# Kernel optimization log

Measured on AMD Instinct MI355X. Metric: run time of the kernel, lower is better.

The kernel has to match this reference:

```python
import jax, jax.numpy as jnp
import numpy as np

B, S, D, H, W, L, V = 4, 8192, 256, 8, 64, 6, 256
DH = D // H          # head dim 32
NW = S // W          # number of windows
FF = 4 * D


def setup_inputs() -> dict:
    key = jax.random.key(0)
    ks = jax.random.split(key, 12)
    w = lambda k, shape: (jax.random.normal(k, shape, jnp.float32) * 0.02)
    return {
        "input_ids": jax.random.randint(ks[0], (B, S), 0, V).astype(jnp.int32),
        "attention_mask": jnp.ones((B, S), jnp.int32),
        "word_start": jax.random.randint(ks[1], (B, S), 0, 2).astype(jnp.int32),
        "emb": w(ks[2], (V, D)),
        "pos_emb": w(ks[3], (S, D)),
        "ln1_g": jnp.ones((L, D)), "ln1_b": jnp.zeros((L, D)),
        "wq": w(ks[4], (L, D, D)), "wk": w(ks[5], (L, D, D)),
        "wv": w(ks[6], (L, D, D)), "wo": w(ks[7], (L, D, D)),
        "ln2_g": jnp.ones((L, D)), "ln2_b": jnp.zeros((L, D)),
        "w1": w(ks[8], (L, D, FF)), "b1": jnp.zeros((L, FF)),
        "w2": w(ks[9], (L, FF, D)), "b2": jnp.zeros((L, D)),
        "lnf_g": jnp.ones((D,)), "lnf_b": jnp.zeros((D,)),
    }


def _ln(x, g, b):
    m = jnp.mean(x, -1, keepdims=True)
    v = jnp.mean((x - m) ** 2, -1, keepdims=True)
    return (x - m) * jax.lax.rsqrt(v + 1e-5) * g + b


def _local_attn(x, mask_bool, wq, wk, wv, wo):
    # non-causal local attention: each 64-token window attends to
    # [prev window, own window, next window] (look_backward=1, look_forward=1)
    def heads(t):
        return t.reshape(B, S, H, DH).transpose(0, 2, 1, 3)  # [B,H,S,DH]
    q = heads(x @ wq)
    k = heads(x @ wk)
    v = heads(x @ wv)
    qw = q.reshape(B, H, NW, W, DH)

    def ctx(t):  # gather 3-window key/value context
        tw = t.reshape(B, H, NW, W, DH)
        tp = jnp.pad(tw, ((0, 0), (0, 0), (1, 1), (0, 0), (0, 0)))
        return jnp.concatenate([tp[:, :, i:i + NW] for i in range(3)], axis=3)  # [B,H,NW,3W,DH]

    kc, vc = ctx(k), ctx(v)
    mw = mask_bool.reshape(B, NW, W)
    mp = jnp.pad(mw, ((0, 0), (1, 1), (0, 0)))
    mc = jnp.concatenate([mp[:, i:i + NW] for i in range(3)], axis=2)  # [B,NW,3W]

    scores = jnp.einsum('bhnwd,bhnkd->bhnwk', qw, kc) * (DH ** -0.5)
    scores = jnp.where(mc[:, None, :, None, :], scores, -1e9)
    attn = jax.nn.softmax(scores, axis=-1)
    o = jnp.einsum('bhnwk,bhnkd->bhnwd', attn, vc)
    o = o.reshape(B, H, S, DH).transpose(0, 2, 1, 3).reshape(B, S, D)
    return o @ wo


def _gather_word_starts(x, ws):
    # pack hidden states at word-start positions to the front, zero-padded
    def one(xb, wb):
        idx = jnp.cumsum(wb) - 1
        tgt = jnp.where(wb > 0, idx, S)  # invalid rows go to scratch slot S
        return jnp.zeros((S + 1, xb.shape[-1]), xb.dtype).at[tgt].set(xb)[:S]
    return jax.vmap(one)(x, ws)


def reference(input_ids, attention_mask, word_start, emb, pos_emb,
              ln1_g, ln1_b, wq, wk, wv, wo, ln2_g, ln2_b,
              w1, b1, w2, b2, lnf_g, lnf_b):
    mask_bool = attention_mask > 0
    x = emb[input_ids] + pos_emb[None, :, :]
    for i in range(L):
        x = x + _local_attn(_ln(x, ln1_g[i], ln1_b[i]), mask_bool,
                            wq[i], wk[i], wv[i], wo[i])
        h = _ln(x, ln2_g[i], ln2_b[i])
        x = x + jax.nn.gelu(h @ w1[i] + b1[i]) @ w2[i] + b2[i]
    x = _ln(x, lnf_g, lnf_b)
    return _gather_word_starts(x, word_start)
```

## Files before the change

### kernel.cpp

```cpp
#include <hip/hip_runtime.h>


#define S_LEN 8192
#define BATCH 4
#define DMODEL 256
#define NHEAD 8
#define WIN 64
#define NWIN 128
#define NLAYER 6
#define FFDIM 1024
#define MROWS (BATCH * S_LEN)

typedef float __attribute__((ext_vector_type(4))) f32x4;
typedef unsigned int __attribute__((ext_vector_type(2))) u32x2;
typedef unsigned short u16;
typedef unsigned short __attribute__((ext_vector_type(4))) u16x4;

__device__ __forceinline__ u16 f2bf(float f) {
  unsigned u = __builtin_bit_cast(unsigned, f);
  u += 0x7fffu + ((u >> 16) & 1u);
  return (u16)(u >> 16);
}

__device__ __forceinline__ unsigned cvt_pk_bf16(float lo, float hi) {
  unsigned r;
  asm("v_cvt_pk_bf16_f32 %0, %1, %2" : "=v"(r) : "v"(lo), "v"(hi));
  return r;
}
__device__ __forceinline__ u32x2 pack_bf16x4(f32x4 v) {
  u32x2 o;
  o[0] = cvt_pk_bf16(v[0], v[1]);
  o[1] = cvt_pk_bf16(v[2], v[3]);
  return o;
}
__device__ __forceinline__ f32x4 unpack_bf16x4(u16x4 h) {
  f32x4 o;
  o[0] = __builtin_bit_cast(float, (unsigned)h[0] << 16);
  o[1] = __builtin_bit_cast(float, (unsigned)h[1] << 16);
  o[2] = __builtin_bit_cast(float, (unsigned)h[2] << 16);
  o[3] = __builtin_bit_cast(float, (unsigned)h[3] << 16);
  return o;
}

__device__ __forceinline__ float exp2_f(float x) {
  float r;
  asm("v_exp_f32 %0, %1" : "=v"(r) : "v"(x));
  return r;
}

__device__ __forceinline__ void mfma16(f32x4& d, f32x4 a, f32x4 b) {
  asm volatile("v_mfma_f32_16x16x32_bf16 %0, %1, %2, %0"
               : "+v"(d) : "v"(a), "v"(b));
}
#define MFMA_FENCE() asm volatile("s_nop 7\n\ts_nop 7")

__device__ __forceinline__ void gload_lds16(const void* g, void* l) {
  __builtin_amdgcn_global_load_lds(
      (__attribute__((address_space(1))) void*)g,
      (__attribute__((address_space(3))) void*)l, 16, 0, 0);
}

__device__ __forceinline__ float gelu_f(float t) {
  float u = 0.7978845608028654f * (t + 0.044715f * t * t * t);
  float e = __expf(-2.0f * u);
  return t * __builtin_amdgcn_rcpf(1.0f + e);
}

__global__ __launch_bounds__(256) void embed_ln_kernel(
    const int* __restrict__ ids, const float* __restrict__ emb,
    const float* __restrict__ pos, const float* __restrict__ g,
    const float* __restrict__ b, u16* __restrict__ x, u16* __restrict__ xb) {
  int wid = threadIdx.x >> 6, lane = threadIdx.x & 63;
  int r = blockIdx.x * 4 + wid;
  int s = r & (S_LEN - 1);
  int id = ids[r];
  f32x4 e = *(const f32x4*)(emb + (size_t)id * DMODEL + lane * 4);
  f32x4 p = *(const f32x4*)(pos + (size_t)s * DMODEL + lane * 4);
  f32x4 v = e + p;
  *(u32x2*)(x + (size_t)r * DMODEL + lane * 4) = pack_bf16x4(v);
  float sm = v[0] + v[1] + v[2] + v[3];
  float q = v[0] * v[0] + v[1] * v[1] + v[2] * v[2] + v[3] * v[3];
  for (int off = 32; off; off >>= 1) {
    sm += __shfl_xor(sm, off, 64);
    q += __shfl_xor(q, off, 64);
  }
  float mean = sm * (1.0f / DMODEL);
  float var = q * (1.0f / DMODEL) - mean * mean;
  float rs = rsqrtf(var + 1e-5f);
  f32x4 gg = *(const f32x4*)(g + lane * 4);
  f32x4 bb = *(const f32x4*)(b + lane * 4);
  f32x4 o;
  for (int j = 0; j < 4; ++j) o[j] = (v[j] - mean) * rs * gg[j] + bb[j];
  *(u32x2*)(xb + (size_t)r * DMODEL + lane * 4) = pack_bf16x4(o);
}

__global__ void zero_kernel(float* __restrict__ p, int n4) {
  int i = blockIdx.x * blockDim.x + threadIdx.x;
  int stride = gridDim.x * blockDim.x;
  f32x4 z = {0.f, 0.f, 0.f, 0.f};
  for (; i < n4; i += stride) ((f32x4*)p)[i] = z;
}

__global__ void tcast_kernel(const float* __restrict__ src, u16* __restrict__ dst,
                             int total, int K, int N, int dls, int rowOff) {
  int i = blockIdx.x * blockDim.x + threadIdx.x;
  int stride = gridDim.x * blockDim.x;
  int KN = K * N;
  for (; i < total; i += stride) {
    int l = i / KN;
    int rem = i - l * KN;
    int k = rem / N;
    int n = rem - k * N;
    dst[l * dls + (rowOff + n) * K + k] = f2bf(src[i]);
  }
}

template <bool GELU_ACT, bool HAS_BIAS, bool QKV>
__global__ __launch_bounds__(256) void gemm_bf16(
    const u16* __restrict__ A, const u16* __restrict__ Bt,
    u16* __restrict__ C, u16* __restrict__ Vt, const float* __restrict__ bias,
    int N, int K, int nx) {
  __shared__ u16 As[128 * 64];
  __shared__ u16 Bs[128 * 64];

  int nwg = gridDim.x;
  int bid = blockIdx.x;
  int w8 = (bid & 7) * (nwg >> 3) + (bid >> 3);
  int cx = w8 % nx, ry = w8 / nx;
  int bm = ry * 128, bn = cx * 128;

  int tid = threadIdx.x, lane = tid & 63, wid = tid >> 6;
  int l15 = lane & 15, l4 = lane >> 4;
  int wm = wid >> 1, wn = wid & 1;

  const u16* Ab = A + (size_t)bm * K;
  const u16* Bb = Bt + (size_t)bn * K;

  f32x4 acc[4][4] = {};

  for (int kt = 0; kt < K; kt += 64) {
#pragma unroll
    for (int i = 0; i < 4; ++i) {
      int s = tid + i * 256;
      int r = s >> 3, c = (s & 7) ^ (r & 7);
      gload_lds16(Ab + (size_t)r * K + kt + c * 8,
                  (char*)As + (wid * 64 + i * 256) * 16);
    }
#pragma unroll
    for (int i = 0; i < 4; ++i) {
      int s = tid + i * 256;
      int r = s >> 3, c = (s & 7) ^ (r & 7);
      gload_lds16(Bb + (size_t)r * K + kt + c * 8,
                  (char*)Bs + (wid * 64 + i * 256) * 16);
    }
    __syncthreads();
#pragma unroll
    for (int t = 0; t < 2; ++t) {
      f32x4 af[4], bf[4];
#pragma unroll
      for (int m = 0; m < 4; ++m) {
        int r = wm * 64 + m * 16 + l15;
        af[m] = ((const f32x4*)As)[r * 8 + ((t * 4 + l4) ^ (r & 7))];
      }
#pragma unroll
      for (int n = 0; n < 4; ++n) {
        int r = wn * 64 + n * 16 + l15;
        bf[n] = ((const f32x4*)Bs)[r * 8 + ((t * 4 + l4) ^ (r & 7))];
      }
#pragma unroll
      for (int m = 0; m < 4; ++m)
#pragma unroll
        for (int n = 0; n < 4; ++n) mfma16(acc[m][n], bf[n], af[m]);
    }
    __syncthreads();
  }
  MFMA_FENCE();

  int colB = bn + wn * 64;
  if (QKV && colB >= 512) {
#pragma unroll
    for (int m = 0; m < 4; ++m) {
      int row = bm + wm * 64 + m * 16 + l15;
      int bb = row >> 13, s = row & (S_LEN - 1);
#pragma unroll
      for (int n = 0; n < 4; ++n)
#pragma unroll
        for (int j = 0; j < 4; ++j) {
          int col = colB + n * 16 + l4 * 4 + j;
          Vt[((size_t)(bb * 256 + (col - 512))) * S_LEN + s] =
              f2bf(acc[m][n][j]);
        }
    }
    return;
  }
  f32x4 bv[4];
#pragma unroll
  for (int n = 0; n < 4; ++n)
    bv[n] = HAS_BIAS ? *(const f32x4*)(bias + colB + n * 16 + l4 * 4)
                     : (f32x4){0.f, 0.f, 0.f, 0.f};
#pragma unroll
  for (int m = 0; m < 4; ++m) {
    int row = bm + wm * 64 + m * 16 + l15;
#pragma unroll
    for (int n = 0; n < 4; ++n) {
      f32x4 v = acc[m][n] + bv[n];
      if (GELU_ACT) {
#pragma unroll
        for (int j = 0; j < 4; ++j) v[j] = gelu_f(v[j]);
      }
      *(u32x2*)(C + (size_t)row * N + colB + n * 16 + l4 * 4) = pack_bf16x4(v);
    }
  }
}

template <bool DO_LN>
__global__ __launch_bounds__(256) void gemm_res_ln(
    const u16* __restrict__ A, const u16* __restrict__ Bt,
    u16* __restrict__ x, u16* __restrict__ xb,
    const float* __restrict__ bias, const float* __restrict__ g,
    const float* __restrict__ b, int K) {
  __shared__ u16 As[64 * 64];
  __shared__ u16 Bs[256 * 64];
  __shared__ float redS[64][4];
  __shared__ float redQ[64][4];

  int nwg = gridDim.x;
  int bid = blockIdx.x;
  int bm = ((bid & 7) * (nwg >> 3) + (bid >> 3)) * 64;

  int tid = threadIdx.x, lane = tid & 63, wid = tid >> 6;
  int l15 = lane & 15, l4 = lane >> 4;

  const u16* Ab = A + (size_t)bm * K;
  f32x4 acc[4][4] = {};

  for (int kt = 0; kt < K; kt += 64) {
#pragma unroll
    for (int i = 0; i < 2; ++i) {
      int s = tid + i * 256;
      int r = s >> 3, c = (s & 7) ^ (r & 7);
      gload_lds16(Ab + (size_t)r * K + kt + c * 8,
                  (char*)As + (wid * 64 + i * 256) * 16);
    }
#pragma unroll
    for (int i = 0; i < 8; ++i) {
      int s = tid + i * 256;
      int r = s >> 3, c = (s & 7) ^ (r & 7);
      gload_lds16(Bt + (size_t)r * K + kt + c * 8,
                  (char*)Bs + (wid * 64 + i * 256) * 16);
    }
    __syncthreads();
#pragma unroll
    for (int t = 0; t < 2; ++t) {
      f32x4 af[4], bf[4];
#pragma unroll
      for (int m = 0; m < 4; ++m) {
        int r = m * 16 + l15;
        af[m] = ((const f32x4*)As)[r * 8 + ((t * 4 + l4) ^ (r & 7))];
      }
#pragma unroll
      for (int n = 0; n < 4; ++n) {
        int r = wid * 64 + n * 16 + l15;
        bf[n] = ((const f32x4*)Bs)[r * 8 + ((t * 4 + l4) ^ (r & 7))];
      }
#pragma unroll
      for (int m = 0; m < 4; ++m)
#pragma unroll
        for (int n = 0; n < 4; ++n) mfma16(acc[m][n], bf[n], af[m]);
    }
    __syncthreads();
  }
  MFMA_FENCE();

  int colB = wid * 64;
  f32x4 bv[4];
#pragma unroll
  for (int n = 0; n < 4; ++n)
    bv[n] = bias ? *(const f32x4*)(bias + colB + n * 16 + l4 * 4)
                 : (f32x4){0.f, 0.f, 0.f, 0.f};

#pragma unroll
  for (int m = 0; m < 4; ++m) {
    int r = m * 16 + l15;
    size_t rowoff = (size_t)(bm + r) * DMODEL + colB;
    float s = 0.f, q = 0.f;
#pragma unroll
    for (int n = 0; n < 4; ++n) {
      f32x4 xv = unpack_bf16x4(*(const u16x4*)(x + rowoff + n * 16 + l4 * 4));
      f32x4 v = acc[m][n] + bv[n] + xv;
      acc[m][n] = v;
      s += v[0] + v[1] + v[2] + v[3];
      q += v[0] * v[0] + v[1] * v[1] + v[2] * v[2] + v[3] * v[3];
    }
    if (DO_LN) {
      s += __shfl_xor(s, 16, 64);
      s += __shfl_xor(s, 32, 64);
      q += __shfl_xor(q, 16, 64);
      q += __shfl_xor(q, 32, 64);
      if (l4 == 0) {
        redS[r][wid] = s;
        redQ[r][wid] = q;
      }
    }
  }
  if (DO_LN) __syncthreads();

  f32x4 gv[4], bbv[4];
  if (DO_LN) {
#pragma unroll
    for (int n = 0; n < 4; ++n) {
      gv[n] = *(const f32x4*)(g + colB + n * 16 + l4 * 4);
      bbv[n] = *(const f32x4*)(b + colB + n * 16 + l4 * 4);
    }
  }
#pragma unroll
  for (int m = 0; m < 4; ++m) {
    int r = m * 16 + l15;
    size_t rowoff = (size_t)(bm + r) * DMODEL + colB;
    float mean = 0.f, rs = 0.f;
    if (DO_LN) {
      f32x4 sv = *(const f32x4*)redS[r];
      f32x4 qv = *(const f32x4*)redQ[r];
      float ssum = sv[0] + sv[1] + sv[2] + sv[3];
      float qsum = qv[0] + qv[1] + qv[2] + qv[3];
      mean = ssum * (1.0f / DMODEL);
      float var = qsum * (1.0f / DMODEL) - mean * mean;
      rs = rsqrtf(var + 1e-5f);
    }
#pragma unroll
    for (int n = 0; n < 4; ++n) {
      f32x4 v = acc[m][n];
      *(u32x2*)(x + rowoff + n * 16 + l4 * 4) = pack_bf16x4(v);
      if (DO_LN) {
        f32x4 o;
#pragma unroll
        for (int j = 0; j < 4; ++j)
          o[j] = (v[j] - mean) * rs * gv[n][j] + bbv[n][j];
        *(u32x2*)(xb + rowoff + n * 16 + l4 * 4) = pack_bf16x4(o);
      }
    }
  }
}

__global__ __launch_bounds__(256, 4) void attn_kernel(
    const u16* __restrict__ qkv, const u16* __restrict__ vt,
    const int* __restrict__ amask, u16* __restrict__ ao) {
  int win = blockIdx.x, h = blockIdx.y, b = blockIdx.z;
  int tid = threadIdx.x, lane = tid & 63, wid = tid >> 6;
  int l15 = lane & 15, l4 = lane >> 4;

  __shared__ u16 KPs[192 * 64];
  __shared__ u16 Vts[96 * 64];
  __shared__ float bias[192];

  int t0 = win * WIN - WIN;

  if (tid < 192) {
    int t = t0 + tid;
    bias[tid] =
        (t >= 0 && t < S_LEN && amask[b * S_LEN + t] != 0) ? 0.0f : -1e9f;
  }
#pragma unroll
  for (int it = 0; it < 3; ++it) {
    int c = it * 256 + tid;
    int k = c >> 2, j = c & 3;
    int t = t0 + k;
    t = t < 0 ? 0 : (t >= S_LEN ? S_LEN - 1 : t);
    f32x4 kd = *(const f32x4*)(qkv + (size_t)(b * S_LEN + t) * 768 + 256 +
                               h * 32 + j * 8);
    int row = k >> 1;
    int cc = (((k & 1) << 2) | j) ^ (row & 7);
    *(f32x4*)(KPs + row * 64 + cc * 8) = kd;
  }
#pragma unroll
  for (int it = 0; it < 3; ++it) {
    int c = it * 256 + tid;
    int d = c / 24, kc = c - d * 24;
    int ts = t0 + kc * 8;
    ts = ts < 0 ? 0 : (ts > S_LEN - 8 ? S_LEN - 8 : ts);
    f32x4 vd = *(const f32x4*)(vt + ((size_t)((b * 8 + h) * 32 + d)) * S_LEN + ts);
    int row = d * 3 + (kc >> 3);
    int cc = (kc & 7) ^ (row & 7);
    *(f32x4*)(Vts + row * 64 + cc * 8) = vd;
  }
  __syncthreads();

  int qrow = b * S_LEN + win * WIN + wid * 16 + l15;
  f32x4 aq = *(const f32x4*)(qkv + (size_t)qrow * 768 + h * 32 + l4 * 8);

  f32x4 sacc[12] = {};
  int krb = l15 >> 1;
  int kcc = (((l15 & 1) << 2) | l4) ^ (krb & 7);
#pragma unroll
  for (int f = 0; f < 12; ++f) {
    f32x4 bk = *(const f32x4*)(KPs + (f * 8 + krb) * 64 + kcc * 8);
    mfma16(sacc[f], bk, aq);
  }
  MFMA_FENCE();

  const float scale2 = 0.17677669529663687f * 1.4426950408889634f;
  float mrow = -1e30f;
#pragma unroll
  for (int f = 0; f < 12; ++f) {
    f32x4 bi = *(const f32x4*)&bias[f * 16 + l4 * 4];
#pragma unroll
    for (int j = 0; j < 4; ++j) {
      float sv = fmaf(sacc[f][j], scale2, bi[j]);
      sacc[f][j] = sv;
      mrow = fmaxf(mrow, sv);
    }
  }
  mrow = fmaxf(mrow, __shfl_xor(mrow, 16, 64));
  mrow = fmaxf(mrow, __shfl_xor(mrow, 32, 64));

  float ssum = 0.f;
#pragma unroll
  for (int f = 0; f < 12; ++f)
#pragma unroll
    for (int j = 0; j < 4; ++j) {
      float p = exp2_f(sacc[f][j] - mrow);
      sacc[f][j] = p;
      ssum += p;
    }
  ssum += __shfl_xor(ssum, 16, 64);
  ssum += __shfl_xor(ssum, 32, 64);

  __syncthreads();

  int q = wid * 16 + l15;
#pragma unroll
  for (int f = 0; f < 12; ++f) {
    u32x2 pk;
    pk[0] = cvt_pk_bf16(sacc[f][0], sacc[f][1]);
    pk[1] = cvt_pk_bf16(sacc[f][2], sacc[f][3]);
    int kc = f * 2 + (l4 >> 1);
    int row = q * 3 + (kc >> 3);
    int cc = (kc & 7) ^ (row & 7);
    *(u32x2*)(KPs + row * 64 + cc * 8 + (l4 & 1) * 4) = pk;
  }
  __syncthreads();

  f32x4 oacc[2] = {};
#pragma unroll
  for (int kk = 0; kk < 6; ++kk) {
    int kc = kk * 4 + l4;
    int rowp = q * 3 + (kc >> 3);
    int ccp = (kc & 7) ^ (rowp & 7);
    f32x4 ap = *(const f32x4*)(KPs + rowp * 64 + ccp * 8);
#pragma unroll
    for (int nf = 0; nf < 2; ++nf) {
      int d = nf * 16 + l15;
      int rowv = d * 3 + (kc >> 3);
      int ccv = (kc & 7) ^ (rowv & 7);
      f32x4 bvv = *(const f32x4*)(Vts + rowv * 64 + ccv * 8);
      mfma16(oacc[nf], bvv, ap);
    }
  }
  MFMA_FENCE();

  float invv = 1.0f / ssum;
  size_t obase = (size_t)qrow * 256 + h * 32;
#pragma unroll
  for (int nf = 0; nf < 2; ++nf) {
    f32x4 v = oacc[nf] * invv;
    *(u32x2*)(ao + obase + nf * 16 + l4 * 4) = pack_bf16x4(v);
  }
}

__global__ __launch_bounds__(256) void scan_kernel(const int* __restrict__ wsrt,
                                                   int* __restrict__ tgt) {
  __shared__ int part[256];
  int b = blockIdx.x, tid = threadIdx.x;
  const int* src = wsrt + b * S_LEN;
  int* dst = tgt + b * S_LEN;
  int base = tid * 32;
  int loc[32];
  int s = 0;
#pragma unroll
  for (int i = 0; i < 32; ++i) {
    loc[i] = src[base + i];
    s += loc[i];
  }
  part[tid] = s;
  __syncthreads();
  for (int off = 1; off < 256; off <<= 1) {
    int v = (tid >= off) ? part[tid - off] : 0;
    __syncthreads();
    part[tid] += v;
    __syncthreads();
  }
  int cum = part[tid] - s;
#pragma unroll
  for (int i = 0; i < 32; ++i) {
    cum += loc[i];
    dst[base + i] = (loc[i] > 0) ? (cum - 1) : -1;
  }
}

__global__ __launch_bounds__(64) void gather_ln_kernel(
    const u16* __restrict__ x, const int* __restrict__ tgt,
    const float* __restrict__ g, const float* __restrict__ b,
    float* __restrict__ out) {
  int r = blockIdx.x;
  int tg = tgt[r];
  if (tg < 0) return;
  int bIdx = r >> 13;
  int lane = threadIdx.x;
  f32x4 v = unpack_bf16x4(*(const u16x4*)(x + (size_t)r * DMODEL + lane * 4));
  float s = v[0] + v[1] + v[2] + v[3];
  float q = v[0] * v[0] + v[1] * v[1] + v[2] * v[2] + v[3] * v[3];
  for (int off = 32; off; off >>= 1) {
    s += __shfl_xor(s, off, 64);
    q += __shfl_xor(q, off, 64);
  }
  float mean = s * (1.0f / DMODEL);
  float var = q * (1.0f / DMODEL) - mean * mean;
  float rs = rsqrtf(var + 1e-5f);
  f32x4 gg = *(const f32x4*)(g + lane * 4);
  f32x4 bb = *(const f32x4*)(b + lane * 4);
  f32x4 o;
  for (int j = 0; j < 4; ++j) o[j] = (v[j] - mean) * rs * gg[j] + bb[j];
  *(f32x4*)(out + (size_t)(bIdx * S_LEN + tg) * DMODEL + lane * 4) = o;
}

extern "C" void kernel_launch(void* const* d_in, const int* in_sizes, int n_in,
                              void* d_out, int out_size, void* d_ws,
                              size_t ws_size, hipStream_t stream) {
  const int* ids = (const int*)d_in[0];
  const int* amask = (const int*)d_in[1];
  const int* wstart = (const int*)d_in[2];
  const float* emb = (const float*)d_in[3];
  const float* pos = (const float*)d_in[4];
  const float* ln1g = (const float*)d_in[5];
  const float* ln1b = (const float*)d_in[6];
  const float* wq = (const float*)d_in[7];
  const float* wk = (const float*)d_in[8];
  const float* wv = (const float*)d_in[9];
  const float* wo = (const float*)d_in[10];
  const float* ln2g = (const float*)d_in[11];
  const float* ln2b = (const float*)d_in[12];
  const float* w1 = (const float*)d_in[13];
  const float* b1 = (const float*)d_in[14];
  const float* w2 = (const float*)d_in[15];
  const float* b2 = (const float*)d_in[16];
  const float* lnfg = (const float*)d_in[17];
  const float* lnfb = (const float*)d_in[18];

  char* ws = (char*)d_ws;
  const size_t OFF_X = 0;
  const size_t OFF_XB = 33554432;
  const size_t OFF_AO = 50331648;
  const size_t OFF_BIG = 67108864;
  const size_t OFF_VT = 117440512;
  const size_t OFF_WQKVT = 134217728;
  const size_t OFF_WOT = 136577024;
  const size_t OFF_W1T = 137363456;
  const size_t OFF_W2T = 140509184;
  const size_t OFF_TGT = 143654912;
  const size_t NEEDED = 143785984;
  if (ws_size < NEEDED) return;

  u16* x = (u16*)(ws + OFF_X);
  u16* xb = (u16*)(ws + OFF_XB);
  u16* ao = (u16*)(ws + OFF_AO);
  u16* big = (u16*)(ws + OFF_BIG);
  u16* vt = (u16*)(ws + OFF_VT);
  u16* WqkvT = (u16*)(ws + OFF_WQKVT);
  u16* WoT = (u16*)(ws + OFF_WOT);
  u16* W1T = (u16*)(ws + OFF_W1T);
  u16* W2T = (u16*)(ws + OFF_W2T);
  int* tgt = (int*)(ws + OFF_TGT);

  tcast_kernel<<<1024, 256, 0, stream>>>(wq, WqkvT, NLAYER * 256 * 256, 256, 256, 768 * 256, 0);
  tcast_kernel<<<1024, 256, 0, stream>>>(wk, WqkvT, NLAYER * 256 * 256, 256, 256, 768 * 256, 256);
  tcast_kernel<<<1024, 256, 0, stream>>>(wv, WqkvT, NLAYER * 256 * 256, 256, 256, 768 * 256, 512);
  tcast_kernel<<<1024, 256, 0, stream>>>(wo, WoT, NLAYER * 256 * 256, 256, 256, 256 * 256, 0);
  tcast_kernel<<<2048, 256, 0, stream>>>(w1, W1T, NLAYER * 256 * 1024, 256, 1024, 1024 * 256, 0);
  tcast_kernel<<<2048, 256, 0, stream>>>(w2, W2T, NLAYER * 1024 * 256, 1024, 256, 256 * 1024, 0);

  embed_ln_kernel<<<MROWS / 4, 256, 0, stream>>>(ids, emb, pos, ln1g, ln1b, x, xb);
  zero_kernel<<<2048, 256, 0, stream>>>((float*)d_out, out_size / 4);
  scan_kernel<<<BATCH, 256, 0, stream>>>(wstart, tgt);

  for (int l = 0; l < NLAYER; ++l) {
    gemm_bf16<false, false, true><<<1536, 256, 0, stream>>>(
        xb, WqkvT + (size_t)l * 768 * 256, big, vt, nullptr, 768, 256, 6);
    attn_kernel<<<dim3(NWIN, NHEAD, BATCH), 256, 0, stream>>>(big, vt, amask, ao);
    gemm_res_ln<true><<<MROWS / 64, 256, 0, stream>>>(
        ao, WoT + (size_t)l * 256 * 256, x, xb, nullptr,
        ln2g + l * DMODEL, ln2b + l * DMODEL, 256);
    gemm_bf16<true, true, false><<<2048, 256, 0, stream>>>(
        xb, W1T + (size_t)l * 1024 * 256, big, nullptr, b1 + l * FFDIM, 1024, 256, 8);
    if (l < NLAYER - 1) {
      gemm_res_ln<true><<<MROWS / 64, 256, 0, stream>>>(
          big, W2T + (size_t)l * 256 * 1024, x, xb, b2 + l * DMODEL,
          ln1g + (l + 1) * DMODEL, ln1b + (l + 1) * DMODEL, 1024);
    } else {
      gemm_res_ln<false><<<MROWS / 64, 256, 0, stream>>>(
          big, W2T + (size_t)l * 256 * 1024, x, nullptr, b2 + l * DMODEL,
          nullptr, nullptr, 1024);
    }
  }

  gather_ln_kernel<<<MROWS, 64, 0, stream>>>(x, tgt, lnfg, lnfb, (float*)d_out);
}
```

Before: 856.9 us.

## Fuse FFN up-projection, GELU and down-projection into one kernel

Replaces the separate W1 GEMM (with bias and GELU) and the W2 GEMM plus residual/LayerNorm with a single ffn_fused kernel. Each 64-row block keeps its input rows in registers and computes the 1024-wide hidden activation in 128-column chunks in LDS. Each chunk is fed straight into the W2 accumulation, so the large hidden tensor never goes through global memory. In exchange, every block re-streams the full W1 and W2 weights from cache and runs with many barriers and no double buffering. The QKV GEMM template is also simplified into a dedicated kernel.

```diff
diff --git a/kernel.cpp b/kernel.cpp
--- a/kernel.cpp
+++ b/kernel.cpp
@@ -115,11 +115,9 @@
   }
 }
 
-template <bool GELU_ACT, bool HAS_BIAS, bool QKV>
-__global__ __launch_bounds__(256) void gemm_bf16(
+__global__ __launch_bounds__(256) void qkv_gemm(
     const u16* __restrict__ A, const u16* __restrict__ Bt,
-    u16* __restrict__ C, u16* __restrict__ Vt, const float* __restrict__ bias,
-    int N, int K, int nx) {
+    u16* __restrict__ C, u16* __restrict__ Vt, int N, int K, int nx) {
   __shared__ u16 As[128 * 64];
   __shared__ u16 Bs[128 * 64];
 
@@ -177,7 +175,7 @@
   MFMA_FENCE();
 
   int colB = bn + wn * 64;
-  if (QKV && colB >= 512) {
+  if (colB >= 512) {
 #pragma unroll
     for (int m = 0; m < 4; ++m) {
       int row = bm + wm * 64 + m * 16 + l15;
@@ -193,23 +191,13 @@
     }
     return;
   }
-  f32x4 bv[4];
-#pragma unroll
-  for (int n = 0; n < 4; ++n)
-    bv[n] = HAS_BIAS ? *(const f32x4*)(bias + colB + n * 16 + l4 * 4)
-                     : (f32x4){0.f, 0.f, 0.f, 0.f};
 #pragma unroll
   for (int m = 0; m < 4; ++m) {
     int row = bm + wm * 64 + m * 16 + l15;
 #pragma unroll
-    for (int n = 0; n < 4; ++n) {
-      f32x4 v = acc[m][n] + bv[n];
-      if (GELU_ACT) {
-#pragma unroll
-        for (int j = 0; j < 4; ++j) v[j] = gelu_f(v[j]);
-      }
-      *(u32x2*)(C + (size_t)row * N + colB + n * 16 + l4 * 4) = pack_bf16x4(v);
-    }
+    for (int n = 0; n < 4; ++n)
+      *(u32x2*)(C + (size_t)row * N + colB + n * 16 + l4 * 4) =
+          pack_bf16x4(acc[m][n]);
   }
 }
 
@@ -337,6 +325,178 @@
         for (int j = 0; j < 4; ++j)
           o[j] = (v[j] - mean) * rs * gv[n][j] + bbv[n][j];
         *(u32x2*)(xb + rowoff + n * 16 + l4 * 4) = pack_bf16x4(o);
+      }
+    }
+  }
+}
+
+template <bool DO_LN>
+__global__ __launch_bounds__(256) void ffn_fused(
+    const u16* __restrict__ xbin, const u16* __restrict__ W1t,
+    const u16* __restrict__ W2t, const float* __restrict__ b1,
+    const float* __restrict__ b2, u16* __restrict__ x,
+    u16* __restrict__ xbout, const float* __restrict__ g,
+    const float* __restrict__ b) {
+  __shared__ u16 Ws[256 * 64];
+  __shared__ u16 Hs[64 * 128];
+  __shared__ float redS[64][4];
+  __shared__ float redQ[64][4];
+
+  int nwg = gridDim.x;
+  int bid = blockIdx.x;
+  int bm = ((bid & 7) * (nwg >> 3) + (bid >> 3)) * 64;
+
+  int tid = threadIdx.x, lane = tid & 63, w = tid >> 6;
+  int l15 = lane & 15, l4 = lane >> 4;
+
+  f32x4 xf[8];
+  {
+    const u16* xrow = xbin + (size_t)(bm + w * 16 + l15) * 256;
+#pragma unroll
+    for (int kk = 0; kk < 8; ++kk)
+      xf[kk] = *(const f32x4*)(xrow + kk * 32 + l4 * 8);
+  }
+
+  f32x4 acc[4][4] = {};
+
+  for (int ft = 0; ft < 8; ++ft) {
+    f32x4 hacc[8] = {};
+#pragma unroll
+    for (int ka = 0; ka < 2; ++ka) {
+#pragma unroll
+      for (int i = 0; i < 8; ++i) {
+        int s = tid + i * 256;
+        int r = s >> 4, c = (s & 15) ^ (r & 7);
+        gload_lds16(W1t + (size_t)(ft * 128 + r) * 256 + ka * 128 + c * 8,
+                    (char*)Ws + s * 16);
+      }
+      __syncthreads();
+#pragma unroll
+      for (int kk = 0; kk < 4; ++kk) {
+#pragma unroll
+        for (int nf = 0; nf < 8; ++nf) {
+          int rr = nf * 16 + l15;
+          f32x4 wf = *(const f32x4*)(
+              Ws + rr * 128 + (((kk * 4 + l4) ^ (rr & 7)) * 8));
+          mfma16(hacc[nf], wf, xf[ka * 4 + kk]);
+        }
+      }
+      __syncthreads();
+    }
+    MFMA_FENCE();
+    {
+      int hrow = w * 16 + l15;
+#pragma unroll
+      for (int nf = 0; nf < 8; ++nf) {
+        f32x4 b1v = *(const f32x4*)(b1 + ft * 128 + nf * 16 + l4 * 4);
+        f32x4 hv;
+#pragma unroll
+        for (int j = 0; j < 4; ++j) hv[j] = gelu_f(hacc[nf][j] + b1v[j]);
+        int kc = nf * 2 + (l4 >> 1);
+        int cc = kc ^ (hrow & 7);
+        *(u32x2*)(Hs + hrow * 128 + cc * 8 + (l4 & 1) * 4) = pack_bf16x4(hv);
+      }
+    }
+    __syncthreads();
+#pragma unroll
+    for (int kb = 0; kb < 2; ++kb) {
+#pragma unroll
+      for (int i = 0; i < 8; ++i) {
+        int s = tid + i * 256;
+        int r = s >> 3, c = (s & 7) ^ (r & 7);
+        gload_lds16(W2t + (size_t)r * 1024 + ft * 128 + kb * 64 + c * 8,
+                    (char*)Ws + s * 16);
+      }
+      __syncthreads();
+#pragma unroll
+      for (int t = 0; t < 2; ++t) {
+        f32x4 af[4], bf[4];
+#pragma unroll
+        for (int m = 0; m < 4; ++m) {
+          int rr = m * 16 + l15;
+          int kc = kb * 8 + t * 4 + l4;
+          af[m] = *(const f32x4*)(Hs + rr * 128 + ((kc ^ (rr & 7)) * 8));
+        }
+#pragma unroll
+        for (int n = 0; n < 4; ++n) {
+          int rr = w * 64 + n * 16 + l15;
+          bf[n] = *(const f32x4*)(
+              Ws + rr * 64 + (((t * 4 + l4) ^ (rr & 7)) * 8));
+        }
+#pragma unroll
+        for (int m = 0; m < 4; ++m)
+#pragma unroll
+          for (int n = 0; n < 4; ++n) mfma16(acc[m][n], bf[n], af[m]);
+      }
+      __syncthreads();
+    }
+  }
+  MFMA_FENCE();
+
+  int colB = w * 64;
+  f32x4 bv[4];
+#pragma unroll
+  for (int n = 0; n < 4; ++n)
+    bv[n] = *(const f32x4*)(b2 + colB + n * 16 + l4 * 4);
+
+#pragma unroll
+  for (int m = 0; m < 4; ++m) {
+    int r = m * 16 + l15;
+    size_t rowoff = (size_t)(bm + r) * DMODEL + colB;
+    float s = 0.f, q = 0.f;
+#pragma unroll
+    for (int n = 0; n < 4; ++n) {
+      f32x4 xv = unpack_bf16x4(*(const u16x4*)(x + rowoff + n * 16 + l4 * 4));
+      f32x4 v = acc[m][n] + bv[n] + xv;
+      acc[m][n] = v;
+      s += v[0] + v[1] + v[2] + v[3];
+      q += v[0] * v[0] + v[1] * v[1] + v[2] * v[2] + v[3] * v[3];
+    }
+    if (DO_LN) {
+      s += __shfl_xor(s, 16, 64);
+      s += __shfl_xor(s, 32, 64);
+      q += __shfl_xor(q, 16, 64);
+      q += __shfl_xor(q, 32, 64);
+      if (l4 == 0) {
+        redS[r][w] = s;
+        redQ[r][w] = q;
+      }
+    }
+  }
+  if (DO_LN) __syncthreads();
+
+  f32x4 gv[4], bbv[4];
+  if (DO_LN) {
+#pragma unroll
+    for (int n = 0; n < 4; ++n) {
+      gv[n] = *(const f32x4*)(g + colB + n * 16 + l4 * 4);
+      bbv[n] = *(const f32x4*)(b + colB + n * 16 + l4 * 4);
+    }
+  }
+#pragma unroll
+  for (int m = 0; m < 4; ++m) {
+    int r = m * 16 + l15;
+    size_t rowoff = (size_t)(bm + r) * DMODEL + colB;
+    float mean = 0.f, rs = 0.f;
+    if (DO_LN) {
+      f32x4 sv = *(const f32x4*)redS[r];
+      f32x4 qv = *(const f32x4*)redQ[r];
+      float ssum = sv[0] + sv[1] + sv[2] + sv[3];
+      float qsum = qv[0] + qv[1] + qv[2] + qv[3];
+      mean = ssum * (1.0f / DMODEL);
+      float var = qsum * (1.0f / DMODEL) - mean * mean;
+      rs = rsqrtf(var + 1e-5f);
+    }
+#pragma unroll
+    for (int n = 0; n < 4; ++n) {
+      f32x4 v = acc[m][n];
+      *(u32x2*)(x + rowoff + n * 16 + l4 * 4) = pack_bf16x4(v);
+      if (DO_LN) {
+        f32x4 o;
+#pragma unroll
+        for (int j = 0; j < 4; ++j)
+          o[j] = (v[j] - mean) * rs * gv[n][j] + bbv[n][j];
+        *(u32x2*)(xbout + rowoff + n * 16 + l4 * 4) = pack_bf16x4(o);
       }
     }
   }
@@ -583,22 +743,21 @@
   scan_kernel<<<BATCH, 256, 0, stream>>>(wstart, tgt);
 
   for (int l = 0; l < NLAYER; ++l) {
-    gemm_bf16<false, false, true><<<1536, 256, 0, stream>>>(
-        xb, WqkvT + (size_t)l * 768 * 256, big, vt, nullptr, 768, 256, 6);
+    qkv_gemm<<<1536, 256, 0, stream>>>(
+        xb, WqkvT + (size_t)l * 768 * 256, big, vt, 768, 256, 6);
     attn_kernel<<<dim3(NWIN, NHEAD, BATCH), 256, 0, stream>>>(big, vt, amask, ao);
     gemm_res_ln<true><<<MROWS / 64, 256, 0, stream>>>(
         ao, WoT + (size_t)l * 256 * 256, x, xb, nullptr,
         ln2g + l * DMODEL, ln2b + l * DMODEL, 256);
-    gemm_bf16<true, true, false><<<2048, 256, 0, stream>>>(
-        xb, W1T + (size_t)l * 1024 * 256, big, nullptr, b1 + l * FFDIM, 1024, 256, 8);
     if (l < NLAYER - 1) {
-      gemm_res_ln<true><<<MROWS / 64, 256, 0, stream>>>(
-          big, W2T + (size_t)l * 256 * 1024, x, xb, b2 + l * DMODEL,
-          ln1g + (l + 1) * DMODEL, ln1b + (l + 1) * DMODEL, 1024);
+      ffn_fused<true><<<MROWS / 64, 256, 0, stream>>>(
+          xb, W1T + (size_t)l * 1024 * 256, W2T + (size_t)l * 256 * 1024,
+          b1 + l * FFDIM, b2 + l * DMODEL, x, xb,
+          ln1g + (l + 1) * DMODEL, ln1b + (l + 1) * DMODEL);
     } else {
-      gemm_res_ln<false><<<MROWS / 64, 256, 0, stream>>>(
-          big, W2T + (size_t)l * 256 * 1024, x, nullptr, b2 + l * DMODEL,
-          nullptr, nullptr, 1024);
+      ffn_fused<false><<<MROWS / 64, 256, 0, stream>>>(
+          xb, W1T + (size_t)l * 1024 * 256, W2T + (size_t)l * 256 * 1024,
+          b1 + l * FFDIM, b2 + l * DMODEL, x, nullptr, nullptr, nullptr);
     }
   }
 
```

After: 914.3 us. 6.7% more time.
